# Kernel optimization log

Measured on AMD Instinct MI355X. Metric: run time of the kernel, lower is better.

The kernel has to match this reference:

```python
import jax, jax.numpy as jnp
import numpy as np

P_DROP = 0.2
THRESH = 1.0


def _conv(x, w, b):
    # NCHW x OIHW, stride 1, padding SAME (k=3, pad=1)
    y = jax.lax.conv_general_dilated(x, w, (1, 1), 'SAME',
                                     dimension_numbers=('NCHW', 'OIHW', 'NCHW'))
    return y + b[None, :, None, None]


def _pool2(x):
    B, C, H, W = x.shape
    return x.reshape(B, C, H // 2, 2, W // 2, 2).mean(axis=(3, 5))


def _lif(inp, mem):
    # integrate-and-fire with soft reset: mem += input; spike if mem >= THRESH
    mem = mem + inp
    spk = (mem >= THRESH).astype(mem.dtype)
    mem = mem - spk * THRESH
    return spk, mem


def _mask(key, shape):
    u = jax.random.uniform(key, shape)
    return jnp.where(u >= P_DROP, 1.0 / (1.0 - P_DROP), 0.0).astype(jnp.float32)


def setup_inputs() -> dict:
    key = jax.random.key(0)
    ks = jax.random.split(key, 16)
    B = 32
    f32 = jnp.float32
    inp = {
        'X': jax.random.uniform(ks[0], (B, 3, 32, 32), dtype=f32),
        'conv1_w': jax.random.normal(ks[1], (64, 3, 3, 3), f32) * np.sqrt(2.0 / (3 * 3 * 64)),
        'conv1_b': jnp.zeros((64,), f32),
        'conv2_w': jax.random.normal(ks[2], (128, 64, 3, 3), f32) * np.sqrt(2.0 / (3 * 3 * 128)),
        'conv2_b': jnp.zeros((128,), f32),
        'conv3_w': jax.random.normal(ks[3], (128, 128, 3, 3), f32) * np.sqrt(2.0 / (3 * 3 * 128)),
        'conv3_b': jnp.zeros((128,), f32),
        'fc1_w': jax.random.normal(ks[4], (1024, 8192), f32) * 0.01,
        'fc1_b': jnp.zeros((1024,), f32),
        'fc2_w': jax.random.normal(ks[5], (10, 1024), f32) * 0.01,
        'fc2_b': jnp.zeros((10,), f32),
        'mask_f1': _mask(ks[6], (B, 64, 32, 32)),
        'mask_f2': _mask(ks[7], (B, 128, 16, 16)),
        'mask_c1': _mask(ks[8], (B, 1024)),
        'timesteps': 8,
    }
    return inp


def reference(X, conv1_w, conv1_b, conv2_w, conv2_b, conv3_w, conv3_b,
              fc1_w, fc1_b, fc2_w, fc2_b, mask_f1, mask_f2, mask_c1, timesteps):
    B = X.shape[0]
    f32 = X.dtype
    m1 = jnp.zeros((B, 64, 32, 32), f32)
    m2 = jnp.zeros((B, 128, 32, 32), f32)
    m3 = jnp.zeros((B, 128, 16, 16), f32)
    c1 = jnp.zeros((B, 1024), f32)
    c2 = jnp.zeros((B, 10), f32)

    def step(carry, _):
        m1, m2, m3, c1, c2 = carry
        s, m1 = _lif(_conv(X, conv1_w, conv1_b), m1)
        s = s * mask_f1
        s, m2 = _lif(_conv(s, conv2_w, conv2_b), m2)
        s = _pool2(s)
        s, m3 = _lif(_conv(s, conv3_w, conv3_b), m3)
        s = s * mask_f2
        s = _pool2(s)
        s = s.reshape(B, -1)  # [B, 8192]
        s, c1 = _lif(s @ fc1_w.T + fc1_b, c1)
        s = s * mask_c1
        s, c2 = _lif(s @ fc2_w.T + fc2_b, c2)
        return (m1, m2, m3, c1, c2), None

    (m1, m2, m3, c1, c2), _ = jax.lax.scan(step, (m1, m2, m3, c1, c2), None,
                                           length=int(timesteps))
    # original returns the final membrane potential of the last Linear layer
    return c2
```

## Files before the change

### kernel.cpp

```cpp
#include <hip/hip_runtime.h>

#define T_STEPS 8

#define N_L1 (32*64*32*32)
#define N_S1P (32*64*34*34)
#define N_M2 (32*128*32*32)
#define N_P2P (32*128*18*20)
#define N_M3 (32*128*16*16)
#define N_P3 (32*8192)
#define N_C1 (32*1024)
#define N_C2 (32*10)

#define OFF_A1  0
#define OFF_M1  (OFF_A1 + N_L1)
#define OFF_S1P (OFF_M1 + N_L1)
#define OFF_M2  (OFF_S1P + N_S1P)
#define OFF_P2P (OFF_M2 + N_M2)
#define OFF_M3  (OFF_P2P + N_P2P)
#define OFF_P3  (OFF_M3 + N_M3)
#define OFF_C1  (OFF_P3 + N_P3)
#define OFF_SF1 (OFF_C1 + N_C1)
#define OFF_C2  (OFF_SF1 + N_C1)
#define N_STATE (N_L1 + N_S1P + N_M2 + N_P2P + N_M3 + N_P3 + 2*N_C1 + N_C2)

__global__ __launch_bounds__(256) void k_conv1(const float* __restrict__ X,
    const float* __restrict__ w, const float* __restrict__ bias,
    float* __restrict__ A1) {
  int idx = blockIdx.x * 256 + threadIdx.x;
  int x = idx & 31, y = (idx >> 5) & 31, oc = (idx >> 10) & 63, b = idx >> 16;
  float acc = bias[oc];
  for (int ic = 0; ic < 3; ++ic) {
    const float* xp = X + (b*3 + ic)*1024;
    const float* wp = w + (oc*3 + ic)*9;
    #pragma unroll
    for (int dy = 0; dy < 3; ++dy) {
      int iy = y + dy - 1;
      if (iy < 0 || iy > 31) continue;
      #pragma unroll
      for (int dx = 0; dx < 3; ++dx) {
        int ix = x + dx - 1;
        if (ix < 0 || ix > 31) continue;
        acc = fmaf(xp[iy*32 + ix], wp[dy*3 + dx], acc);
      }
    }
  }
  A1[idx] = acc;
}

__global__ __launch_bounds__(256) void k_lif1(const float4* __restrict__ A1,
    const float4* __restrict__ mask, float4* __restrict__ m1,
    float* __restrict__ s1pad) {
  int i = blockIdx.x * 256 + threadIdx.x;
  float4 m = m1[i], a = A1[i], k = mask[i];
  int x4 = (i & 7) * 4;
  int y  = (i >> 3) & 31;
  int plane = i >> 8;
  float* dst = s1pad + (size_t)plane*1156 + (y + 1)*34 + (x4 + 1);
  float p;
  m.x += a.x; p = (m.x >= 1.0f) ? 1.0f : 0.0f; m.x -= p; dst[0] = p * k.x;
  m.y += a.y; p = (m.y >= 1.0f) ? 1.0f : 0.0f; m.y -= p; dst[1] = p * k.y;
  m.z += a.z; p = (m.z >= 1.0f) ? 1.0f : 0.0f; m.z -= p; dst[2] = p * k.z;
  m.w += a.w; p = (m.w >= 1.0f) ? 1.0f : 0.0f; m.w -= p; dst[3] = p * k.w;
  m1[i] = m;
}

__global__ __launch_bounds__(256, 4) void k_conv2(const float* __restrict__ s1pad,
    const float* __restrict__ w, const float* __restrict__ bias,
    float* __restrict__ m2, float* __restrict__ p2pad) {
  int bid = blockIdx.x;
  int ocg = bid & 15;
  int yt  = (bid >> 4) & 1;
  int b   = bid >> 5;
  int t = threadIdx.x;
  int xp = t & 15, ty = t >> 4;

  __shared__ float lds[8 * 612];
  float acc[2][8];
  #pragma unroll
  for (int o = 0; o < 8; ++o) { acc[0][o] = 0.f; acc[1][o] = 0.f; }

  for (int chunk = 0; chunk < 8; ++chunk) {
    const float* srcp = s1pad + (size_t)(b*64 + chunk*8)*1156 + yt*544;
    __syncthreads();
    #pragma unroll
    for (int ic = 0; ic < 8; ++ic) {
      const float4* s4 = (const float4*)(srcp + ic*1156);
      float4* d4 = (float4*)(lds + ic*612);
      for (int j4 = t; j4 < 153; j4 += 256)
        d4[j4] = s4[j4];
    }
    __syncthreads();
    const float* wc = w + ((size_t)(ocg*8)*64 + chunk*8)*9;
    for (int ic = 0; ic < 8; ++ic) {
      float in12[12];
      const float* lp = &lds[ic*612 + ty*34 + 2*xp];
      #pragma unroll
      for (int dy = 0; dy < 3; ++dy)
        #pragma unroll
        for (int dx = 0; dx < 4; ++dx)
          in12[dy*4+dx] = lp[dy*34 + dx];
      #pragma unroll
      for (int o = 0; o < 8; ++o) {
        const float* wp = wc + (o*64 + ic)*9;
        #pragma unroll
        for (int k = 0; k < 9; ++k) {
          const int dy = k/3, dx = k - 3*(k/3);
          acc[0][o] = fmaf(in12[dy*4+dx],   wp[k], acc[0][o]);
          acc[1][o] = fmaf(in12[dy*4+dx+1], wp[k], acc[1][o]);
        }
      }
    }
  }

  int y = yt*16 + ty;
  int x0 = 2*xp;
  bool ywriter = ((ty & 1) == 0);
  #pragma unroll
  for (int o = 0; o < 8; ++o) {
    int oc = ocg*8 + o;
    size_t mi = (size_t)(b*128 + oc)*1024 + y*32 + x0;
    float2 mv = *(const float2*)&m2[mi];
    float ma = mv.x + acc[0][o] + bias[oc];
    float mb = mv.y + acc[1][o] + bias[oc];
    float sa = (ma >= 1.0f) ? 1.0f : 0.0f;
    float sb = (mb >= 1.0f) ? 1.0f : 0.0f;
    float2 mo; mo.x = ma - sa; mo.y = mb - sb;
    *(float2*)&m2[mi] = mo;
    float s = sa + sb;
    s += __shfl_xor(s, 16);
    if (ywriter)
      p2pad[(size_t)(b*128 + oc)*360 + ((y>>1) + 1)*20 + (xp + 1)] = s * 0.25f;
  }
}

__global__ __launch_bounds__(512, 4) void k_conv3(const float* __restrict__ p2pad,
    const float* __restrict__ w, const float* __restrict__ bias,
    const float* __restrict__ mf2, float* __restrict__ m3, float* __restrict__ p3) {
  int ocq = blockIdx.x & 15;
  int b   = blockIdx.x >> 4;
  int t = threadIdx.x;
  int xp = t & 7, y = (t >> 3) & 15, oh = t >> 8;
  int ocb = __builtin_amdgcn_readfirstlane(ocq*8 + oh*4);

  __shared__ float lds[8 * 360];
  float acc[2][4];
  #pragma unroll
  for (int o = 0; o < 4; ++o) { acc[0][o] = 0.f; acc[1][o] = 0.f; }

  for (int chunk = 0; chunk < 16; ++chunk) {
    const float4* srcp4 = (const float4*)(p2pad + (size_t)(b*128 + chunk*8)*360);
    __syncthreads();
    for (int j4 = t; j4 < 720; j4 += 512)
      ((float4*)lds)[j4] = srcp4[j4];
    __syncthreads();
    const float* wc = w + ((size_t)ocb*128 + chunk*8)*9;
    for (int ic = 0; ic < 8; ++ic) {
      float in12[12];
      const float* lp = &lds[ic*360 + y*20 + 2*xp];
      #pragma unroll
      for (int dy = 0; dy < 3; ++dy)
        #pragma unroll
        for (int dx = 0; dx < 4; ++dx)
          in12[dy*4+dx] = lp[dy*20 + dx];
      #pragma unroll
      for (int o = 0; o < 4; ++o) {
        const float* wp = wc + (o*128 + ic)*9;
        #pragma unroll
        for (int k = 0; k < 9; ++k) {
          const int dy = k/3, dx = k - 3*(k/3);
          acc[0][o] = fmaf(in12[dy*4+dx],   wp[k], acc[0][o]);
          acc[1][o] = fmaf(in12[dy*4+dx+1], wp[k], acc[1][o]);
        }
      }
    }
  }

  int x0 = 2*xp;
  bool ywriter = ((y & 1) == 0);
  #pragma unroll
  for (int o = 0; o < 4; ++o) {
    int oc = ocb + o;
    size_t base = (size_t)(b*128 + oc)*256 + y*16 + x0;
    float2 mv = *(const float2*)&m3[base];
    float2 fv = *(const float2*)&mf2[base];
    float ma = mv.x + acc[0][o] + bias[oc];
    float mb = mv.y + acc[1][o] + bias[oc];
    float sa = (ma >= 1.0f) ? 1.0f : 0.0f;
    float sb = (mb >= 1.0f) ? 1.0f : 0.0f;
    float2 mo; mo.x = ma - sa; mo.y = mb - sb;
    *(float2*)&m3[base] = mo;
    float s = sa * fv.x + sb * fv.y;
    s += __shfl_xor(s, 8);
    if (ywriter)
      p3[(size_t)b*8192 + oc*64 + (y>>1)*8 + xp] = s * 0.25f;
  }
}

__global__ __launch_bounds__(128) void k_fc1v4(const float* __restrict__ p3,
    const float* __restrict__ w, const float* __restrict__ bias,
    const float* __restrict__ mask, float* __restrict__ c1, float* __restrict__ sf1) {
  const float4* w4  = (const float4*)w;
  const float4* p34 = (const float4*)p3;
  int ug = blockIdx.x >> 1;
  int bg = blockIdx.x & 1;
  int u0 = ug * 8, b0 = bg * 16;
  int t = threadIdx.x;
  int u_l = t & 7, b_sub = t >> 3;

  __shared__ float4 lds4[8*130 + 16*129];
  float4* wl = lds4;
  float4* sl = lds4 + 8*130;

  float acc = 0.f;
  for (int kc = 0; kc < 16; ++kc) {
    __syncthreads();
    #pragma unroll
    for (int j0 = 0; j0 < 1024; j0 += 128) {
      int j = j0 + t;
      int u_i = j >> 7, k4 = j & 127;
      wl[u_i*130 + k4] = w4[(size_t)(u0 + u_i)*2048 + kc*128 + k4];
    }
    #pragma unroll
    for (int j0 = 0; j0 < 2048; j0 += 128) {
      int j = j0 + t;
      int b_i = j >> 7, k4 = j & 127;
      sl[b_i*129 + k4] = p34[(size_t)(b0 + b_i)*2048 + kc*128 + k4];
    }
    __syncthreads();
    const float4* wp = wl + u_l*130;
    const float4* sp = sl + b_sub*129;
    #pragma unroll 8
    for (int k4 = 0; k4 < 128; ++k4) {
      float4 wv = wp[k4];
      float4 sv = sp[k4];
      acc = fmaf(wv.x, sv.x, acc);
      acc = fmaf(wv.y, sv.y, acc);
      acc = fmaf(wv.z, sv.z, acc);
      acc = fmaf(wv.w, sv.w, acc);
    }
  }

  int u = u0 + u_l, b = b0 + b_sub;
  int mi = b * 1024 + u;
  float m = c1[mi] + acc + bias[u];
  float spk = (m >= 1.0f) ? 1.0f : 0.0f;
  c1[mi] = m - spk;
  sf1[mi] = spk * mask[mi];
}

__global__ __launch_bounds__(256) void k_fc2(const float* __restrict__ sf1,
    const float* __restrict__ w, const float* __restrict__ bias,
    float* __restrict__ c2, float* __restrict__ out) {
  int idx = blockIdx.x * 256 + threadIdx.x;
  if (idx >= 320) return;
  int u = idx >> 5;
  int b = idx & 31;
  const float4* wp = (const float4*)(w + u * 1024);
  const float4* sp = (const float4*)(sf1 + b * 1024);
  float acc = 0.f;
  #pragma unroll 4
  for (int i = 0; i < 256; ++i) {
    float4 a = wp[i];
    float4 s = sp[i];
    acc = fmaf(a.x, s.x, acc);
    acc = fmaf(a.y, s.y, acc);
    acc = fmaf(a.z, s.z, acc);
    acc = fmaf(a.w, s.w, acc);
  }
  int mi = b * 10 + u;
  float m = c2[mi] + acc + bias[u];
  float spk = (m >= 1.0f) ? 1.0f : 0.0f;
  m -= spk;
  c2[mi] = m;
  out[mi] = m;
}

extern "C" void kernel_launch(void* const* d_in, const int* in_sizes, int n_in,
                              void* d_out, int out_size, void* d_ws, size_t ws_size,
                              hipStream_t stream) {
  const float* X   = (const float*)d_in[0];
  const float* w1  = (const float*)d_in[1];
  const float* b1  = (const float*)d_in[2];
  const float* w2  = (const float*)d_in[3];
  const float* b2  = (const float*)d_in[4];
  const float* w3  = (const float*)d_in[5];
  const float* b3  = (const float*)d_in[6];
  const float* fw1 = (const float*)d_in[7];
  const float* fb1 = (const float*)d_in[8];
  const float* fw2 = (const float*)d_in[9];
  const float* fb2 = (const float*)d_in[10];
  const float* mf1 = (const float*)d_in[11];
  const float* mf2 = (const float*)d_in[12];
  const float* mc1 = (const float*)d_in[13];
  float* out = (float*)d_out;

  float* ws    = (float*)d_ws;
  float* A1    = ws + OFF_A1;
  float* m1    = ws + OFF_M1;
  float* s1pad = ws + OFF_S1P;
  float* m2    = ws + OFF_M2;
  float* p2pad = ws + OFF_P2P;
  float* m3    = ws + OFF_M3;
  float* p3    = ws + OFF_P3;
  float* c1    = ws + OFF_C1;
  float* sf1   = ws + OFF_SF1;
  float* c2    = ws + OFF_C2;

  hipMemsetAsync(m1, 0, (size_t)(N_STATE - N_L1) * 4, stream);

  k_conv1<<<N_L1/256, 256, 0, stream>>>(X, w1, b1, A1);

  for (int t = 0; t < T_STEPS; ++t) {
    k_lif1<<<N_L1/4/256, 256, 0, stream>>>((const float4*)A1, (const float4*)mf1,
                                           (float4*)m1, s1pad);
    k_conv2<<<1024, 256, 0, stream>>>(s1pad, w2, b2, m2, p2pad);
    k_conv3<<<512, 512, 0, stream>>>(p2pad, w3, b3, mf2, m3, p3);
    k_fc1v4<<<256, 128, 0, stream>>>(p3, fw1, fb1, mc1, c1, sf1);
    k_fc2<<<2, 256, 0, stream>>>(sf1, fw2, fb2, c2, out);
  }
}
```

Measured before the change: 2.021 ms.

## Split conv3 by half-image rows, one output pixel per thread

The conv3 kernel now launches 1024 blocks of 256 threads, each covering half of the image rows for 8 output channels, instead of 512 blocks of 512 threads covering the full image. Each thread computes one output pixel rather than two adjacent ones, and the pooling reduction uses two shuffles. This raises block count and shrinks the LDS tile (8×200 floats), aiming for better occupancy and more parallelism. In exchange, each thread loads 9 inputs per channel for one output instead of 12 for two, so input reuse drops. The halo rows are also loaded twice across the two row blocks.

After: 1.953 ms. 1.03x faster.

```diff
diff --git a/kernel.cpp b/kernel.cpp
--- a/kernel.cpp
+++ b/kernel.cpp
@@ -133,66 +133,64 @@
   }
 }
 
-__global__ __launch_bounds__(512, 4) void k_conv3(const float* __restrict__ p2pad,
+__global__ __launch_bounds__(256, 4) void k_conv3(const float* __restrict__ p2pad,
     const float* __restrict__ w, const float* __restrict__ bias,
     const float* __restrict__ mf2, float* __restrict__ m3, float* __restrict__ p3) {
-  int ocq = blockIdx.x & 15;
-  int b   = blockIdx.x >> 4;
+  int bid = blockIdx.x;
+  int yt  = bid & 1;
+  int ocg = (bid >> 1) & 15;
+  int b   = bid >> 5;
   int t = threadIdx.x;
-  int xp = t & 7, y = (t >> 3) & 15, oh = t >> 8;
-  int ocb = __builtin_amdgcn_readfirstlane(ocq*8 + oh*4);
-
-  __shared__ float lds[8 * 360];
-  float acc[2][4];
+  int x = t & 15, y = (t >> 4) & 7, og2 = t >> 7;
+  int ocb = __builtin_amdgcn_readfirstlane(ocg*8 + og2*4);
+
+  __shared__ float lds[8 * 200];
+  float acc[4];
   #pragma unroll
-  for (int o = 0; o < 4; ++o) { acc[0][o] = 0.f; acc[1][o] = 0.f; }
-
+  for (int o = 0; o < 4; ++o) acc[o] = 0.f;
+
+  int ic_s = t >> 5, r0 = t & 31;
   for (int chunk = 0; chunk < 16; ++chunk) {
-    const float4* srcp4 = (const float4*)(p2pad + (size_t)(b*128 + chunk*8)*360);
-    __syncthreads();
-    for (int j4 = t; j4 < 720; j4 += 512)
-      ((float4*)lds)[j4] = srcp4[j4];
+    const float4* src4 = (const float4*)(p2pad
+        + (size_t)(b*128 + chunk*8 + ic_s)*360 + yt*160);
+    float4* dst4 = (float4*)(lds + ic_s*200);
+    __syncthreads();
+    dst4[r0] = src4[r0];
+    if (r0 < 18) dst4[32 + r0] = src4[32 + r0];
     __syncthreads();
     const float* wc = w + ((size_t)ocb*128 + chunk*8)*9;
     for (int ic = 0; ic < 8; ++ic) {
-      float in12[12];
-      const float* lp = &lds[ic*360 + y*20 + 2*xp];
+      float in9[9];
+      const float* lp = &lds[ic*200 + y*20 + x];
       #pragma unroll
       for (int dy = 0; dy < 3; ++dy)
         #pragma unroll
-        for (int dx = 0; dx < 4; ++dx)
-          in12[dy*4+dx] = lp[dy*20 + dx];
+        for (int dx = 0; dx < 3; ++dx)
+          in9[dy*3+dx] = lp[dy*20 + dx];
       #pragma unroll
       for (int o = 0; o < 4; ++o) {
         const float* wp = wc + (o*128 + ic)*9;
         #pragma unroll
-        for (int k = 0; k < 9; ++k) {
-          const int dy = k/3, dx = k - 3*(k/3);
-          acc[0][o] = fmaf(in12[dy*4+dx],   wp[k], acc[0][o]);
-          acc[1][o] = fmaf(in12[dy*4+dx+1], wp[k], acc[1][o]);
-        }
+        for (int k = 0; k < 9; ++k)
+          acc[o] = fmaf(in9[k], wp[k], acc[o]);
       }
     }
   }
 
-  int x0 = 2*xp;
-  bool ywriter = ((y & 1) == 0);
+  int y_out = yt*8 + y;
+  bool writer = ((x & 1) == 0) && ((y & 1) == 0);
   #pragma unroll
   for (int o = 0; o < 4; ++o) {
     int oc = ocb + o;
-    size_t base = (size_t)(b*128 + oc)*256 + y*16 + x0;
-    float2 mv = *(const float2*)&m3[base];
-    float2 fv = *(const float2*)&mf2[base];
-    float ma = mv.x + acc[0][o] + bias[oc];
-    float mb = mv.y + acc[1][o] + bias[oc];
-    float sa = (ma >= 1.0f) ? 1.0f : 0.0f;
-    float sb = (mb >= 1.0f) ? 1.0f : 0.0f;
-    float2 mo; mo.x = ma - sa; mo.y = mb - sb;
-    *(float2*)&m3[base] = mo;
-    float s = sa * fv.x + sb * fv.y;
-    s += __shfl_xor(s, 8);
-    if (ywriter)
-      p3[(size_t)b*8192 + oc*64 + (y>>1)*8 + xp] = s * 0.25f;
+    size_t base = (size_t)(b*128 + oc)*256 + y_out*16 + x;
+    float m = m3[base] + acc[o] + bias[oc];
+    float spk = (m >= 1.0f) ? 1.0f : 0.0f;
+    m3[base] = m - spk;
+    float s = spk * mf2[base];
+    s += __shfl_xor(s, 1);
+    s += __shfl_xor(s, 16);
+    if (writer)
+      p3[(size_t)b*8192 + oc*64 + (y_out>>1)*8 + (x>>1)] = s * 0.25f;
   }
 }
 
@@ -314,7 +312,7 @@
     k_lif1<<<N_L1/4/256, 256, 0, stream>>>((const float4*)A1, (const float4*)mf1,
                                            (float4*)m1, s1pad);
     k_conv2<<<1024, 256, 0, stream>>>(s1pad, w2, b2, m2, p2pad);
-    k_conv3<<<512, 512, 0, stream>>>(p2pad, w3, b3, mf2, m3, p3);
+    k_conv3<<<1024, 256, 0, stream>>>(p2pad, w3, b3, mf2, m3, p3);
     k_fc1v4<<<256, 128, 0, stream>>>(p3, fw1, fb1, mc1, c1, sf1);
     k_fc2<<<2, 256, 0, stream>>>(sf1, fw2, fb2, c2, out);
   }
```
